# Optimization experiments

Measured on AMD Instinct MI355X. Metric: run time of the kernel, lower is better.

## Reference

```python
import jax, jax.numpy as jnp
import numpy as np

N_HEADS = 16
NEG_BIAS = -1000000000.0


def setup_inputs() -> dict:
    key = jax.random.key(0)
    k1, k2, k3, k4 = jax.random.split(key, 4)
    B, S, D = 2, 2048, 1024
    queries = jax.random.normal(k1, (B, S, D), dtype=jnp.float32)
    keys = jax.random.normal(k2, (B, S, D), dtype=jnp.float32)
    values = jax.random.normal(k3, (B, S, D), dtype=jnp.float32)
    mask = jax.random.randint(k4, (B, S, S), 0, 2, dtype=jnp.int32)
    return {"queries": queries, "keys": keys, "values": values, "mask": mask}


def _split_heads(x):
    B, S, D = x.shape
    return x.reshape(B, S, N_HEADS, D // N_HEADS).transpose(0, 2, 1, 3)  # [B,H,S,d]


def reference(queries, keys, values, mask):
    q = _split_heads(queries)   # [B,H,Sq,d]
    k = _split_heads(keys)      # [B,H,Sk,d]
    v = _split_heads(values)    # [B,H,Sk,d]
    d_head = q.shape[-1]
    # scaled dot product similarity
    sim = jnp.einsum('bhqd,bhkd->bhqk', q, k) / jnp.sqrt(jnp.float32(d_head))
    # additive mask (softmax attention function -> non-hadamard)
    bias = NEG_BIAS * (1.0 - mask.astype(sim.dtype))[:, None]  # [B,1,Sq,Sk]
    sim = sim + bias
    # softmax with max-subtraction (numerically stable, as in original)
    weights = jax.nn.softmax(sim, axis=-1)
    out = jnp.einsum('bhqk,bhkd->bhqd', weights, v)  # [B,H,Sq,d]
    B, H, Sq, d = out.shape
    return out.transpose(0, 2, 1, 3).reshape(B, Sq, H * d)
```

## Files before the change

### kernel.cpp

```cpp
#include <hip/hip_runtime.h>

#define S_LEN 2048
#define D_MODEL 1024
#define DH 64
#define BQ 128
#define BK 128
#define LDK 72
#define LDV 136
#define ZSCALE 0.18033688f

using short8 = __attribute__((ext_vector_type(8))) short;
using s4v    = __attribute__((ext_vector_type(4))) short;
using f32x4  = __attribute__((ext_vector_type(4))) float;

__device__ __forceinline__ unsigned short f2bf(float x) {
    union { float f; unsigned int u; } c; c.f = x;
    unsigned int u = c.u;
    u += 0x7fffu + ((u >> 16) & 1u);
    return (unsigned short)(u >> 16);
}

__global__ __launch_bounds__(256) void cvt_fused(const float* __restrict__ V,
                                                 const int* __restrict__ M,
                                                 const float* __restrict__ K,
                                                 unsigned short* __restrict__ VT,
                                                 unsigned long long* __restrict__ Mb,
                                                 unsigned short* __restrict__ KB) {
    const int blk = blockIdx.x;
    const int tid = threadIdx.x;
    if (blk < 1024) {
        __shared__ float tsF[64][65];
        const int b  = blk >> 9;
        const int h  = (blk >> 5) & 15;
        const int s0 = (blk & 31) * 64;
        #pragma unroll
        for (int it = 0; it < 2; ++it) {
            int seg = tid + it * 256;
            int s = seg >> 3, d8 = (seg & 7) << 3;
            const float* p = V + (size_t)(b * S_LEN + s0 + s) * D_MODEL + h * DH + d8;
            f32x4 a = *(const f32x4*)p;
            f32x4 c = *(const f32x4*)(p + 4);
            #pragma unroll
            for (int j = 0; j < 4; ++j) { tsF[s][d8 + j] = a[j]; tsF[s][d8 + 4 + j] = c[j]; }
        }
        __syncthreads();
        #pragma unroll
        for (int it = 0; it < 2; ++it) {
            int seg = tid + it * 256;
            int d = seg >> 3, s8 = (seg & 7) << 3;
            short8 w;
            #pragma unroll
            for (int j = 0; j < 8; ++j) w[j] = (short)f2bf(tsF[s8 + j][d]);
            *(short8*)(VT + ((size_t)((b * 16 + h) * 64 + d)) * S_LEN + s0 + s8) = w;
        }
    } else if (blk < 2048) {
        const int pb   = blk - 1024;
        const int wave = tid >> 6, lane = tid & 63;
        const int row  = pb * 4 + wave;
        const int* mp  = M + (size_t)row * S_LEN;
        #pragma unroll 4
        for (int it = 0; it < 32; ++it) {
            int m = mp[it * 64 + lane];
            unsigned long long bal = __ballot(m != 0);
            if (lane == 0) Mb[(size_t)row * 32 + it] = bal;
        }
    } else {
        size_t base = (size_t)(blk - 2048) * 4096;
        #pragma unroll
        for (int it = 0; it < 4; ++it) {
            size_t i = base + ((size_t)(it * 256 + tid)) * 4;
            f32x4 a = *(const f32x4*)(K + i);
            s4v w;
            #pragma unroll
            for (int j = 0; j < 4; ++j) w[j] = (short)f2bf(a[j]);
            *(s4v*)(KB + i) = w;
        }
    }
}

__global__ __launch_bounds__(256) void mha_fwd_v11(
    const float* __restrict__ Q,
    const float* __restrict__ K,
    const unsigned short* __restrict__ KB,
    const unsigned short* __restrict__ VT,
    const unsigned long long* __restrict__ Mb,
    float* __restrict__ O,
    int kbf)
{
    __shared__ alignas(16) unsigned short Ks[BK][LDK];
    __shared__ alignas(16) unsigned short Vt[DH][LDV];

    const int blk0 = blockIdx.x;
    const int blk  = ((blk0 & 7) << 6) | (blk0 >> 3);

    const int b   = blk >> 8;
    const int h   = (blk >> 4) & 15;
    const int qbase = (blk & 15) * BQ;
    const int bh  = b * 16 + h;

    const int tid  = threadIdx.x;
    const int wave = tid >> 6;
    const int lane = tid & 63;
    const int n16  = lane & 15;
    const int quad = lane >> 4;
    const int bq   = quad << 3;

    const int srow = tid >> 3, sc8 = (tid & 7) << 3;
    const int prow = (((srow >> 2) & 1) << 4) | (((srow >> 3) & 3) << 2) | (srow & 3);
    const int vrow = tid >> 4, vc8 = (tid & 15) << 3;

    short8 qf[2][2];
    #pragma unroll
    for (int qg = 0; qg < 2; ++qg) {
        const size_t qoff = (size_t)(b * S_LEN + qbase + wave * 32 + qg * 16 + n16) * D_MODEL
                          + h * DH + quad * 8;
        f32x4 a0 = *(const f32x4*)(Q + qoff);
        f32x4 a1 = *(const f32x4*)(Q + qoff + 4);
        f32x4 a2 = *(const f32x4*)(Q + qoff + 32);
        f32x4 a3 = *(const f32x4*)(Q + qoff + 36);
        short8 q0, q1;
        #pragma unroll
        for (int j = 0; j < 4; ++j) {
            q0[j] = (short)f2bf(a0[j] * ZSCALE); q0[4 + j] = (short)f2bf(a1[j] * ZSCALE);
            q1[j] = (short)f2bf(a2[j] * ZSCALE); q1[4 + j] = (short)f2bf(a3[j] * ZSCALE);
        }
        qf[qg][0] = q0; qf[qg][1] = q1;
    }

    const short8 ones = {0x3F80,0x3F80,0x3F80,0x3F80,0x3F80,0x3F80,0x3F80,0x3F80};

    f32x4 o[2][4], o4[2];
    #pragma unroll
    for (int qg = 0; qg < 2; ++qg) {
        #pragma unroll
        for (int dg = 0; dg < 4; ++dg) o[qg][dg] = f32x4{0.f,0.f,0.f,0.f};
        o4[qg] = f32x4{0.f,0.f,0.f,0.f};
    }

    const unsigned long long* mrow[2];
    #pragma unroll
    for (int qg = 0; qg < 2; ++qg)
        mrow[qg] = Mb + (size_t)(b * S_LEN + qbase + wave * 32 + qg * 16 + n16) * 32;

    const size_t kbase = (size_t)(b * S_LEN) * D_MODEL + h * DH;
    const size_t vbase = (size_t)(bh * 64) * S_LEN;

    short8 ka[4], va[4];
    unsigned long long mw[2][2];
    if (kbf) {
        #pragma unroll
        for (int i = 0; i < 4; ++i)
            ka[i] = *(const short8*)(KB + kbase + (size_t)(i * 32 + srow) * D_MODEL + sc8);
    } else {
        #pragma unroll
        for (int i = 0; i < 4; ++i) {
            const float* kp = K + kbase + (size_t)(i * 32 + srow) * D_MODEL + sc8;
            f32x4 p0 = *(const f32x4*)kp, p1 = *(const f32x4*)(kp + 4);
            short8 w;
            #pragma unroll
            for (int j = 0; j < 4; ++j) { w[j] = (short)f2bf(p0[j]); w[4 + j] = (short)f2bf(p1[j]); }
            ka[i] = w;
        }
    }
    #pragma unroll
    for (int i = 0; i < 4; ++i)
        va[i] = *(const short8*)(VT + vbase + (size_t)(vrow + 16 * i) * S_LEN + vc8);
    #pragma unroll
    for (int qg = 0; qg < 2; ++qg) { mw[qg][0] = mrow[qg][0]; mw[qg][1] = mrow[qg][1]; }

    for (int kb = 0; kb < S_LEN; kb += BK) {
        __builtin_amdgcn_s_barrier();
        __builtin_amdgcn_sched_barrier(0);

        #pragma unroll
        for (int i = 0; i < 4; ++i) {
            *(short8*)&Ks[prow + 32 * i][sc8] = ka[i];
            *(short8*)&Vt[vrow + 16 * i][vc8] = va[i];
        }

        const int kn = kb + BK;
        const bool more = kn < S_LEN;
        short8 nka[4], nva[4];
        unsigned long long nmw[2][2];
        if (more) {
            if (kbf) {
                #pragma unroll
                for (int i = 0; i < 4; ++i)
                    nka[i] = *(const short8*)(KB + kbase + (size_t)(kn + i * 32 + srow) * D_MODEL + sc8);
            } else {
                #pragma unroll
                for (int i = 0; i < 4; ++i) {
                    const float* kp = K + kbase + (size_t)(kn + i * 32 + srow) * D_MODEL + sc8;
                    f32x4 p0 = *(const f32x4*)kp, p1 = *(const f32x4*)(kp + 4);
                    short8 w;
                    #pragma unroll
                    for (int j = 0; j < 4; ++j) { w[j] = (short)f2bf(p0[j]); w[4 + j] = (short)f2bf(p1[j]); }
                    nka[i] = w;
                }
            }
            #pragma unroll
            for (int i = 0; i < 4; ++i)
                nva[i] = *(const short8*)(VT + vbase + (size_t)(vrow + 16 * i) * S_LEN + kn + vc8);
            const int wi = kn >> 6;
            #pragma unroll
            for (int qg = 0; qg < 2; ++qg) { nmw[qg][0] = mrow[qg][wi]; nmw[qg][1] = mrow[qg][wi + 1]; }
        }

        asm volatile("s_waitcnt lgkmcnt(0)" ::: "memory");
        __builtin_amdgcn_s_barrier();
        __builtin_amdgcn_sched_barrier(0);

        unsigned int am[2][4];
        #pragma unroll
        for (int qg = 0; qg < 2; ++qg) {
            am[qg][0] = ((unsigned int)mw[qg][0]) >> bq;
            am[qg][1] = ((unsigned int)(mw[qg][0] >> 32)) >> bq;
            am[qg][2] = ((unsigned int)mw[qg][1]) >> bq;
            am[qg][3] = ((unsigned int)(mw[qg][1] >> 32)) >> bq;
        }

        union { unsigned int u[4]; short8 v; } Af[2][4];
        __builtin_amdgcn_s_setprio(1);
        #pragma unroll
        for (int ct = 0; ct < 8; ++ct) {
            short8 kf0 = *(const short8*)&Ks[ct * 16 + n16][     quad * 8];
            short8 kf1 = *(const short8*)&Ks[ct * 16 + n16][32 + quad * 8];
            f32x4 sA = {0.f,0.f,0.f,0.f}, sB = sA;
            sA = __builtin_amdgcn_mfma_f32_16x16x32_bf16(kf0, qf[0][0], sA, 0, 0, 0);
            sA = __builtin_amdgcn_mfma_f32_16x16x32_bf16(kf1, qf[0][1], sA, 0, 0, 0);
            sB = __builtin_amdgcn_mfma_f32_16x16x32_bf16(kf0, qf[1][0], sB, 0, 0, 0);
            sB = __builtin_amdgcn_mfma_f32_16x16x32_bf16(kf1, qf[1][1], sB, 0, 0, 0);
            unsigned int puA[4], puB[4];
            #pragma unroll
            for (int r = 0; r < 4; ++r) {
                puA[r] = __float_as_uint(__builtin_amdgcn_exp2f(sA[r]));
                puB[r] = __float_as_uint(__builtin_amdgcn_exp2f(sB[r]));
            }
            const int sel = ct >> 1, sb = (ct & 1) * 4;
            unsigned int nibA = (am[0][sel] >> sb) & 0xFu;
            unsigned int nibB = (am[1][sel] >> sb) & 0xFu;
            unsigned int m8A = ((nibA * 0x00204081u) & 0x01010101u) * 0xFFu;
            unsigned int m8B = ((nibB * 0x00204081u) & 0x01010101u) * 0xFFu;
            const int kc = ct >> 1, ub = (ct & 1) * 2;
            Af[0][kc].u[ub + 0] = __builtin_amdgcn_perm(puA[1], puA[0], 0x07060302u)
                                & __builtin_amdgcn_perm(0u, m8A, 0x01010000u);
            Af[0][kc].u[ub + 1] = __builtin_amdgcn_perm(puA[3], puA[2], 0x07060302u)
                                & __builtin_amdgcn_perm(0u, m8A, 0x03030202u);
            Af[1][kc].u[ub + 0] = __builtin_amdgcn_perm(puB[1], puB[0], 0x07060302u)
                                & __builtin_amdgcn_perm(0u, m8B, 0x01010000u);
            Af[1][kc].u[ub + 1] = __builtin_amdgcn_perm(puB[3], puB[2], 0x07060302u)
                                & __builtin_amdgcn_perm(0u, m8B, 0x03030202u);
        }

        #pragma unroll
        for (int kc = 0; kc < 4; ++kc) {
            short8 v0 = *(const short8*)&Vt[      n16][kc * 32 + quad * 8];
            short8 v1 = *(const short8*)&Vt[16 + n16][kc * 32 + quad * 8];
            short8 v2 = *(const short8*)&Vt[32 + n16][kc * 32 + quad * 8];
            short8 v3 = *(const short8*)&Vt[48 + n16][kc * 32 + quad * 8];
            #pragma unroll
            for (int qg = 0; qg < 2; ++qg) {
                short8 af = Af[qg][kc].v;
                o[qg][0] = __builtin_amdgcn_mfma_f32_16x16x32_bf16(af, v0, o[qg][0], 0, 0, 0);
                o[qg][1] = __builtin_amdgcn_mfma_f32_16x16x32_bf16(af, v1, o[qg][1], 0, 0, 0);
                o[qg][2] = __builtin_amdgcn_mfma_f32_16x16x32_bf16(af, v2, o[qg][2], 0, 0, 0);
                o[qg][3] = __builtin_amdgcn_mfma_f32_16x16x32_bf16(af, v3, o[qg][3], 0, 0, 0);
                o4[qg]   = __builtin_amdgcn_mfma_f32_16x16x32_bf16(af, ones, o4[qg], 0, 0, 0);
            }
        }
        __builtin_amdgcn_s_setprio(0);

        if (more) {
            #pragma unroll
            for (int i = 0; i < 4; ++i) { ka[i] = nka[i]; va[i] = nva[i]; }
            #pragma unroll
            for (int qg = 0; qg < 2; ++qg) { mw[qg][0] = nmw[qg][0]; mw[qg][1] = nmw[qg][1]; }
        }
    }

    #pragma unroll
    for (int qg = 0; qg < 2; ++qg) {
        #pragma unroll
        for (int r = 0; r < 4; ++r) {
            float rl = 1.f / o4[qg][r];
            size_t row = (size_t)(b * S_LEN + qbase + wave * 32 + qg * 16 + quad * 4 + r);
            float* op = O + row * D_MODEL + h * DH + n16;
            op[0]  = o[qg][0][r] * rl;
            op[16] = o[qg][1][r] * rl;
            op[32] = o[qg][2][r] * rl;
            op[48] = o[qg][3][r] * rl;
        }
    }
}

extern "C" void kernel_launch(void* const* d_in, const int* in_sizes, int n_in,
                              void* d_out, int out_size, void* d_ws, size_t ws_size,
                              hipStream_t stream) {
    const float* Q = (const float*)d_in[0];
    const float* K = (const float*)d_in[1];
    const float* V = (const float*)d_in[2];
    const int*   M = (const int*)d_in[3];
    float*       O = (float*)d_out;

    const size_t NEL = (size_t)2 * S_LEN * D_MODEL;
    const size_t VT_BYTES = NEL * sizeof(unsigned short);
    const size_t KB_BYTES = NEL * sizeof(unsigned short);
    const size_t MB_BYTES = (size_t)2 * S_LEN * 32 * 8;

    if (ws_size >= VT_BYTES + KB_BYTES + MB_BYTES) {
        unsigned short* VT = (unsigned short*)d_ws;
        unsigned short* KB = (unsigned short*)((char*)d_ws + VT_BYTES);
        unsigned long long* Mb = (unsigned long long*)((char*)d_ws + VT_BYTES + KB_BYTES);
        hipLaunchKernelGGL(cvt_fused, dim3(3072), dim3(256), 0, stream, V, M, K, VT, Mb, KB);
        hipLaunchKernelGGL(mha_fwd_v11, dim3(512), dim3(256), 0, stream,
                           Q, K, KB, VT, Mb, O, 1);
    } else {
        unsigned short* VT = (unsigned short*)d_ws;
        unsigned long long* Mb = (unsigned long long*)((char*)d_ws + VT_BYTES);
        hipLaunchKernelGGL(cvt_fused, dim3(2048), dim3(256), 0, stream, V, M, K, VT, Mb, (unsigned short*)0);
        hipLaunchKernelGGL(mha_fwd_v11, dim3(512), dim3(256), 0, stream,
                           Q, K, (const unsigned short*)0, VT, Mb, O, 0);
    }
}
```

Baseline: 171.3 us.

## Load K fragments directly to registers and double-buffer V in LDS

Drops the shared-memory K tile. Each wave now loads its K MFMA fragments straight from global memory into registers, using a row permutation that matches the old LDS layout, and prefetches the next tile after the QK stage. V goes into a two-stage LDS buffer, which lets the loop drop one of its two barriers per iteration. This removes LDS traffic and a barrier for K. In exchange, each wave redundantly reads the whole K tile from global/L2 (4x duplication across waves) and register pressure rises from holding 16 short8 K fragments.

```diff
diff --git a/kernel.cpp b/kernel.cpp
--- a/kernel.cpp
+++ b/kernel.cpp
@@ -5,7 +5,6 @@
 #define DH 64
 #define BQ 128
 #define BK 128
-#define LDK 72
 #define LDV 136
 #define ZSCALE 0.18033688f
 
@@ -78,7 +77,7 @@
     }
 }
 
-__global__ __launch_bounds__(256) void mha_fwd_v11(
+__global__ __launch_bounds__(256) void mha_fwd_v12(
     const float* __restrict__ Q,
     const float* __restrict__ K,
     const unsigned short* __restrict__ KB,
@@ -87,8 +86,7 @@
     float* __restrict__ O,
     int kbf)
 {
-    __shared__ alignas(16) unsigned short Ks[BK][LDK];
-    __shared__ alignas(16) unsigned short Vt[DH][LDV];
+    __shared__ alignas(16) unsigned short Vt[2][DH][LDV];
 
     const int blk0 = blockIdx.x;
     const int blk  = ((blk0 & 7) << 6) | (blk0 >> 3);
@@ -104,9 +102,8 @@
     const int n16  = lane & 15;
     const int quad = lane >> 4;
     const int bq   = quad << 3;
-
-    const int srow = tid >> 3, sc8 = (tid & 7) << 3;
-    const int prow = (((srow >> 2) & 1) << 4) | (((srow >> 3) & 3) << 2) | (srow & 3);
+    const int lrow = ((n16 >> 2) << 3) | (n16 & 3);
+
     const int vrow = tid >> 4, vc8 = (tid & 15) << 3;
 
     short8 qf[2][2];
@@ -145,59 +142,51 @@
     const size_t kbase = (size_t)(b * S_LEN) * D_MODEL + h * DH;
     const size_t vbase = (size_t)(bh * 64) * S_LEN;
 
-    short8 ka[4], va[4];
+    short8 kf[8][2];
+    auto load_kf = [&](int kt) {
+        #pragma unroll
+        for (int ct = 0; ct < 8; ++ct) {
+            const int cst  = ((ct >> 2) << 6) | (((ct >> 1) & 1) << 5) | ((ct & 1) << 2);
+            const int crow = kt + cst + lrow;
+            if (kbf) {
+                const unsigned short* kp = KB + kbase + (size_t)crow * D_MODEL + quad * 8;
+                kf[ct][0] = *(const short8*)kp;
+                kf[ct][1] = *(const short8*)(kp + 32);
+            } else {
+                const float* kp = K + kbase + (size_t)crow * D_MODEL + quad * 8;
+                f32x4 p0 = *(const f32x4*)kp,        p1 = *(const f32x4*)(kp + 4);
+                f32x4 p2 = *(const f32x4*)(kp + 32), p3 = *(const f32x4*)(kp + 36);
+                short8 w0, w1;
+                #pragma unroll
+                for (int j = 0; j < 4; ++j) {
+                    w0[j] = (short)f2bf(p0[j]); w0[4 + j] = (short)f2bf(p1[j]);
+                    w1[j] = (short)f2bf(p2[j]); w1[4 + j] = (short)f2bf(p3[j]);
+                }
+                kf[ct][0] = w0; kf[ct][1] = w1;
+            }
+        }
+    };
+
+    short8 va[4];
     unsigned long long mw[2][2];
-    if (kbf) {
-        #pragma unroll
-        for (int i = 0; i < 4; ++i)
-            ka[i] = *(const short8*)(KB + kbase + (size_t)(i * 32 + srow) * D_MODEL + sc8);
-    } else {
-        #pragma unroll
-        for (int i = 0; i < 4; ++i) {
-            const float* kp = K + kbase + (size_t)(i * 32 + srow) * D_MODEL + sc8;
-            f32x4 p0 = *(const f32x4*)kp, p1 = *(const f32x4*)(kp + 4);
-            short8 w;
-            #pragma unroll
-            for (int j = 0; j < 4; ++j) { w[j] = (short)f2bf(p0[j]); w[4 + j] = (short)f2bf(p1[j]); }
-            ka[i] = w;
-        }
-    }
     #pragma unroll
     for (int i = 0; i < 4; ++i)
         va[i] = *(const short8*)(VT + vbase + (size_t)(vrow + 16 * i) * S_LEN + vc8);
+    load_kf(0);
     #pragma unroll
     for (int qg = 0; qg < 2; ++qg) { mw[qg][0] = mrow[qg][0]; mw[qg][1] = mrow[qg][1]; }
 
-    for (int kb = 0; kb < S_LEN; kb += BK) {
-        __builtin_amdgcn_s_barrier();
-        __builtin_amdgcn_sched_barrier(0);
-
-        #pragma unroll
-        for (int i = 0; i < 4; ++i) {
-            *(short8*)&Ks[prow + 32 * i][sc8] = ka[i];
-            *(short8*)&Vt[vrow + 16 * i][vc8] = va[i];
-        }
+    int p = 0;
+    for (int kb = 0; kb < S_LEN; kb += BK, p ^= 1) {
+        #pragma unroll
+        for (int i = 0; i < 4; ++i)
+            *(short8*)&Vt[p][vrow + 16 * i][vc8] = va[i];
 
         const int kn = kb + BK;
         const bool more = kn < S_LEN;
-        short8 nka[4], nva[4];
+        short8 nva[4];
         unsigned long long nmw[2][2];
         if (more) {
-            if (kbf) {
-                #pragma unroll
-                for (int i = 0; i < 4; ++i)
-                    nka[i] = *(const short8*)(KB + kbase + (size_t)(kn + i * 32 + srow) * D_MODEL + sc8);
-            } else {
-                #pragma unroll
-                for (int i = 0; i < 4; ++i) {
-                    const float* kp = K + kbase + (size_t)(kn + i * 32 + srow) * D_MODEL + sc8;
-                    f32x4 p0 = *(const f32x4*)kp, p1 = *(const f32x4*)(kp + 4);
-                    short8 w;
-                    #pragma unroll
-                    for (int j = 0; j < 4; ++j) { w[j] = (short)f2bf(p0[j]); w[4 + j] = (short)f2bf(p1[j]); }
-                    nka[i] = w;
-                }
-            }
             #pragma unroll
             for (int i = 0; i < 4; ++i)
                 nva[i] = *(const short8*)(VT + vbase + (size_t)(vrow + 16 * i) * S_LEN + kn + vc8);
@@ -205,10 +194,6 @@
             #pragma unroll
             for (int qg = 0; qg < 2; ++qg) { nmw[qg][0] = mrow[qg][wi]; nmw[qg][1] = mrow[qg][wi + 1]; }
         }
-
-        asm volatile("s_waitcnt lgkmcnt(0)" ::: "memory");
-        __builtin_amdgcn_s_barrier();
-        __builtin_amdgcn_sched_barrier(0);
 
         unsigned int am[2][4];
         #pragma unroll
@@ -223,13 +208,11 @@
         __builtin_amdgcn_s_setprio(1);
         #pragma unroll
         for (int ct = 0; ct < 8; ++ct) {
-            short8 kf0 = *(const short8*)&Ks[ct * 16 + n16][     quad * 8];
-            short8 kf1 = *(const short8*)&Ks[ct * 16 + n16][32 + quad * 8];
             f32x4 sA = {0.f,0.f,0.f,0.f}, sB = sA;
-            sA = __builtin_amdgcn_mfma_f32_16x16x32_bf16(kf0, qf[0][0], sA, 0, 0, 0);
-            sA = __builtin_amdgcn_mfma_f32_16x16x32_bf16(kf1, qf[0][1], sA, 0, 0, 0);
-            sB = __builtin_amdgcn_mfma_f32_16x16x32_bf16(kf0, qf[1][0], sB, 0, 0, 0);
-            sB = __builtin_amdgcn_mfma_f32_16x16x32_bf16(kf1, qf[1][1], sB, 0, 0, 0);
+            sA = __builtin_amdgcn_mfma_f32_16x16x32_bf16(kf[ct][0], qf[0][0], sA, 0, 0, 0);
+            sA = __builtin_amdgcn_mfma_f32_16x16x32_bf16(kf[ct][1], qf[0][1], sA, 0, 0, 0);
+            sB = __builtin_amdgcn_mfma_f32_16x16x32_bf16(kf[ct][0], qf[1][0], sB, 0, 0, 0);
+            sB = __builtin_amdgcn_mfma_f32_16x16x32_bf16(kf[ct][1], qf[1][1], sB, 0, 0, 0);
             unsigned int puA[4], puB[4];
             #pragma unroll
             for (int r = 0; r < 4; ++r) {
@@ -251,13 +234,21 @@
             Af[1][kc].u[ub + 1] = __builtin_amdgcn_perm(puB[3], puB[2], 0x07060302u)
                                 & __builtin_amdgcn_perm(0u, m8B, 0x03030202u);
         }
-
+        __builtin_amdgcn_s_setprio(0);
+
+        asm volatile("s_waitcnt lgkmcnt(0)" ::: "memory");
+        __builtin_amdgcn_s_barrier();
+        __builtin_amdgcn_sched_barrier(0);
+
+        if (more) load_kf(kn);
+
+        __builtin_amdgcn_s_setprio(1);
         #pragma unroll
         for (int kc = 0; kc < 4; ++kc) {
-            short8 v0 = *(const short8*)&Vt[      n16][kc * 32 + quad * 8];
-            short8 v1 = *(const short8*)&Vt[16 + n16][kc * 32 + quad * 8];
-            short8 v2 = *(const short8*)&Vt[32 + n16][kc * 32 + quad * 8];
-            short8 v3 = *(const short8*)&Vt[48 + n16][kc * 32 + quad * 8];
+            short8 v0 = *(const short8*)&Vt[p][      n16][kc * 32 + quad * 8];
+            short8 v1 = *(const short8*)&Vt[p][16 + n16][kc * 32 + quad * 8];
+            short8 v2 = *(const short8*)&Vt[p][32 + n16][kc * 32 + quad * 8];
+            short8 v3 = *(const short8*)&Vt[p][48 + n16][kc * 32 + quad * 8];
             #pragma unroll
             for (int qg = 0; qg < 2; ++qg) {
                 short8 af = Af[qg][kc].v;
@@ -272,7 +263,7 @@
 
         if (more) {
             #pragma unroll
-            for (int i = 0; i < 4; ++i) { ka[i] = nka[i]; va[i] = nva[i]; }
+            for (int i = 0; i < 4; ++i) va[i] = nva[i];
             #pragma unroll
             for (int qg = 0; qg < 2; ++qg) { mw[qg][0] = nmw[qg][0]; mw[qg][1] = nmw[qg][1]; }
         }
@@ -312,13 +303,13 @@
         unsigned short* KB = (unsigned short*)((char*)d_ws + VT_BYTES);
         unsigned long long* Mb = (unsigned long long*)((char*)d_ws + VT_BYTES + KB_BYTES);
         hipLaunchKernelGGL(cvt_fused, dim3(3072), dim3(256), 0, stream, V, M, K, VT, Mb, KB);
-        hipLaunchKernelGGL(mha_fwd_v11, dim3(512), dim3(256), 0, stream,
+        hipLaunchKernelGGL(mha_fwd_v12, dim3(512), dim3(256), 0, stream,
                            Q, K, KB, VT, Mb, O, 1);
     } else {
         unsigned short* VT = (unsigned short*)d_ws;
         unsigned long long* Mb = (unsigned long long*)((char*)d_ws + VT_BYTES);
         hipLaunchKernelGGL(cvt_fused, dim3(2048), dim3(256), 0, stream, V, M, K, VT, Mb, (unsigned short*)0);
-        hipLaunchKernelGGL(mha_fwd_v11, dim3(512), dim3(256), 0, stream,
+        hipLaunchKernelGGL(mha_fwd_v12, dim3(512), dim3(256), 0, stream,
                            Q, K, (const unsigned short*)0, VT, Mb, O, 0);
     }
 }
```

New measurement: 214.6 us. 1.25x slower.

## Software-pipeline QK and PV across tiles with double-buffered LDS

Applied to the files above, without the earlier changes.

Double-buffers the K and V shared-memory tiles. The PV MFMAs of tile t-1 are interleaved with the QK and exp work of tile t, so matrix-core and VALU/transcendental work can overlap within a wave. The main loop is manually unrolled by two, with ping-pong register sets for K/V/mask prefetch and for the probability fragments. This doubles LDS use and raises register pressure, which could lower occupancy or cause spills.

```diff
diff --git a/kernel.cpp b/kernel.cpp
--- a/kernel.cpp
+++ b/kernel.cpp
@@ -5,6 +5,7 @@
 #define DH 64
 #define BQ 128
 #define BK 128
+#define NT (S_LEN / BK)
 #define LDK 72
 #define LDV 136
 #define ZSCALE 0.18033688f
@@ -12,6 +13,9 @@
 using short8 = __attribute__((ext_vector_type(8))) short;
 using s4v    = __attribute__((ext_vector_type(4))) short;
 using f32x4  = __attribute__((ext_vector_type(4))) float;
+using u32x4  = __attribute__((ext_vector_type(4))) unsigned int;
+
+#define BMM(a, b, c) __builtin_amdgcn_mfma_f32_16x16x32_bf16((a), (b), (c), 0, 0, 0)
 
 __device__ __forceinline__ unsigned short f2bf(float x) {
     union { float f; unsigned int u; } c; c.f = x;
@@ -78,7 +82,7 @@
     }
 }
 
-__global__ __launch_bounds__(256) void mha_fwd_v11(
+__global__ __launch_bounds__(256) void mha_fwd_v13(
     const float* __restrict__ Q,
     const float* __restrict__ K,
     const unsigned short* __restrict__ KB,
@@ -87,8 +91,8 @@
     float* __restrict__ O,
     int kbf)
 {
-    __shared__ alignas(16) unsigned short Ks[BK][LDK];
-    __shared__ alignas(16) unsigned short Vt[DH][LDV];
+    __shared__ alignas(16) unsigned short Ks[2][BK][LDK];
+    __shared__ alignas(16) unsigned short Vt[2][DH][LDV];
 
     const int blk0 = blockIdx.x;
     const int blk  = ((blk0 & 7) << 6) | (blk0 >> 3);
@@ -145,72 +149,45 @@
     const size_t kbase = (size_t)(b * S_LEN) * D_MODEL + h * DH;
     const size_t vbase = (size_t)(bh * 64) * S_LEN;
 
-    short8 ka[4], va[4];
-    unsigned long long mw[2][2];
-    if (kbf) {
+    short8 kaA[4], vaA[4], kaB[4], vaB[4];
+    unsigned long long mwA[2][2], mwB[2][2];
+    u32x4 AfA[2][4], AfB[2][4];
+
+    auto LOADKV = [&](int kb2, short8 (&ka)[4], short8 (&va)[4]) {
+        if (kb2 >= S_LEN) return;
+        if (kbf) {
+            #pragma unroll
+            for (int i = 0; i < 4; ++i)
+                ka[i] = *(const short8*)(KB + kbase + (size_t)(kb2 + i * 32 + srow) * D_MODEL + sc8);
+        } else {
+            #pragma unroll
+            for (int i = 0; i < 4; ++i) {
+                const float* kp = K + kbase + (size_t)(kb2 + i * 32 + srow) * D_MODEL + sc8;
+                f32x4 p0 = *(const f32x4*)kp, p1 = *(const f32x4*)(kp + 4);
+                short8 w;
+                #pragma unroll
+                for (int j = 0; j < 4; ++j) { w[j] = (short)f2bf(p0[j]); w[4 + j] = (short)f2bf(p1[j]); }
+                ka[i] = w;
+            }
+        }
         #pragma unroll
         for (int i = 0; i < 4; ++i)
-            ka[i] = *(const short8*)(KB + kbase + (size_t)(i * 32 + srow) * D_MODEL + sc8);
-    } else {
+            va[i] = *(const short8*)(VT + vbase + (size_t)(vrow + 16 * i) * S_LEN + kb2 + vc8);
+    };
+    auto LOADM = [&](int kb2, unsigned long long (&mw)[2][2]) {
+        if (kb2 >= S_LEN) return;
+        const int wi = kb2 >> 6;
+        #pragma unroll
+        for (int qg = 0; qg < 2; ++qg) { mw[qg][0] = mrow[qg][wi]; mw[qg][1] = mrow[qg][wi + 1]; }
+    };
+    auto STAGE = [&](int pb, short8 (&ka)[4], short8 (&va)[4]) {
         #pragma unroll
         for (int i = 0; i < 4; ++i) {
-            const float* kp = K + kbase + (size_t)(i * 32 + srow) * D_MODEL + sc8;
-            f32x4 p0 = *(const f32x4*)kp, p1 = *(const f32x4*)(kp + 4);
-            short8 w;
-            #pragma unroll
-            for (int j = 0; j < 4; ++j) { w[j] = (short)f2bf(p0[j]); w[4 + j] = (short)f2bf(p1[j]); }
-            ka[i] = w;
-        }
-    }
-    #pragma unroll
-    for (int i = 0; i < 4; ++i)
-        va[i] = *(const short8*)(VT + vbase + (size_t)(vrow + 16 * i) * S_LEN + vc8);
-    #pragma unroll
-    for (int qg = 0; qg < 2; ++qg) { mw[qg][0] = mrow[qg][0]; mw[qg][1] = mrow[qg][1]; }
-
-    for (int kb = 0; kb < S_LEN; kb += BK) {
-        __builtin_amdgcn_s_barrier();
-        __builtin_amdgcn_sched_barrier(0);
-
-        #pragma unroll
-        for (int i = 0; i < 4; ++i) {
-            *(short8*)&Ks[prow + 32 * i][sc8] = ka[i];
-            *(short8*)&Vt[vrow + 16 * i][vc8] = va[i];
-        }
-
-        const int kn = kb + BK;
-        const bool more = kn < S_LEN;
-        short8 nka[4], nva[4];
-        unsigned long long nmw[2][2];
-        if (more) {
-            if (kbf) {
-                #pragma unroll
-                for (int i = 0; i < 4; ++i)
-                    nka[i] = *(const short8*)(KB + kbase + (size_t)(kn + i * 32 + srow) * D_MODEL + sc8);
-            } else {
-                #pragma unroll
-                for (int i = 0; i < 4; ++i) {
-                    const float* kp = K + kbase + (size_t)(kn + i * 32 + srow) * D_MODEL + sc8;
-                    f32x4 p0 = *(const f32x4*)kp, p1 = *(const f32x4*)(kp + 4);
-                    short8 w;
-                    #pragma unroll
-                    for (int j = 0; j < 4; ++j) { w[j] = (short)f2bf(p0[j]); w[4 + j] = (short)f2bf(p1[j]); }
-                    nka[i] = w;
-                }
-            }
-            #pragma unroll
-            for (int i = 0; i < 4; ++i)
-                nva[i] = *(const short8*)(VT + vbase + (size_t)(vrow + 16 * i) * S_LEN + kn + vc8);
-            const int wi = kn >> 6;
-            #pragma unroll
-            for (int qg = 0; qg < 2; ++qg) { nmw[qg][0] = mrow[qg][wi]; nmw[qg][1] = mrow[qg][wi + 1]; }
-        }
-
-        asm volatile("s_waitcnt lgkmcnt(0)" ::: "memory");
-        __builtin_amdgcn_s_barrier();
-        __builtin_amdgcn_sched_barrier(0);
-
-        unsigned int am[2][4];
+            *(short8*)&Ks[pb][prow + 32 * i][sc8] = ka[i];
+            *(short8*)&Vt[pb][vrow + 16 * i][vc8] = va[i];
+        }
+    };
+    auto MKAM = [&](unsigned long long (&mw)[2][2], unsigned int (&am)[2][4]) {
         #pragma unroll
         for (int qg = 0; qg < 2; ++qg) {
             am[qg][0] = ((unsigned int)mw[qg][0]) >> bq;
@@ -218,64 +195,108 @@
             am[qg][2] = ((unsigned int)mw[qg][1]) >> bq;
             am[qg][3] = ((unsigned int)(mw[qg][1] >> 32)) >> bq;
         }
-
-        union { unsigned int u[4]; short8 v; } Af[2][4];
+    };
+    auto QKCT = [&](int pb, int ct, unsigned int (&am)[2][4], u32x4 (&Af)[2][4]) {
+        short8 kf0 = *(const short8*)&Ks[pb][ct * 16 + n16][     quad * 8];
+        short8 kf1 = *(const short8*)&Ks[pb][ct * 16 + n16][32 + quad * 8];
+        f32x4 sA = {0.f,0.f,0.f,0.f}, sB = sA;
+        sA = BMM(kf0, qf[0][0], sA); sA = BMM(kf1, qf[0][1], sA);
+        sB = BMM(kf0, qf[1][0], sB); sB = BMM(kf1, qf[1][1], sB);
+        unsigned int puA[4], puB[4];
+        #pragma unroll
+        for (int r = 0; r < 4; ++r) {
+            puA[r] = __float_as_uint(__builtin_amdgcn_exp2f(sA[r]));
+            puB[r] = __float_as_uint(__builtin_amdgcn_exp2f(sB[r]));
+        }
+        const int sel = ct >> 1, sb = (ct & 1) * 4, kc = ct >> 1, ub = (ct & 1) * 2;
+        unsigned int nibA = (am[0][sel] >> sb) & 0xFu;
+        unsigned int nibB = (am[1][sel] >> sb) & 0xFu;
+        unsigned int m8A = ((nibA * 0x00204081u) & 0x01010101u) * 0xFFu;
+        unsigned int m8B = ((nibB * 0x00204081u) & 0x01010101u) * 0xFFu;
+        Af[0][kc][ub + 0] = __builtin_amdgcn_perm(puA[1], puA[0], 0x07060302u)
+                          & __builtin_amdgcn_perm(0u, m8A, 0x01010000u);
+        Af[0][kc][ub + 1] = __builtin_amdgcn_perm(puA[3], puA[2], 0x07060302u)
+                          & __builtin_amdgcn_perm(0u, m8A, 0x03030202u);
+        Af[1][kc][ub + 0] = __builtin_amdgcn_perm(puB[1], puB[0], 0x07060302u)
+                          & __builtin_amdgcn_perm(0u, m8B, 0x01010000u);
+        Af[1][kc][ub + 1] = __builtin_amdgcn_perm(puB[3], puB[2], 0x07060302u)
+                          & __builtin_amdgcn_perm(0u, m8B, 0x03030202u);
+    };
+    auto PVKC = [&](int pb, int kc, u32x4 (&Af)[2][4]) {
+        short8 v0 = *(const short8*)&Vt[pb][      n16][kc * 32 + quad * 8];
+        short8 v1 = *(const short8*)&Vt[pb][16 + n16][kc * 32 + quad * 8];
+        short8 v2 = *(const short8*)&Vt[pb][32 + n16][kc * 32 + quad * 8];
+        short8 v3 = *(const short8*)&Vt[pb][48 + n16][kc * 32 + quad * 8];
+        union { u32x4 u; short8 s; } c0, c1;
+        c0.u = Af[0][kc]; c1.u = Af[1][kc];
+        o[0][0] = BMM(c0.s, v0, o[0][0]); o[0][1] = BMM(c0.s, v1, o[0][1]);
+        o[0][2] = BMM(c0.s, v2, o[0][2]); o[0][3] = BMM(c0.s, v3, o[0][3]);
+        o4[0]   = BMM(c0.s, ones, o4[0]);
+        o[1][0] = BMM(c1.s, v0, o[1][0]); o[1][1] = BMM(c1.s, v1, o[1][1]);
+        o[1][2] = BMM(c1.s, v2, o[1][2]); o[1][3] = BMM(c1.s, v3, o[1][3]);
+        o4[1]   = BMM(c1.s, ones, o4[1]);
+    };
+    auto COMPUTE = [&](int qb, int vb, unsigned int (&am)[2][4],
+                       u32x4 (&AfC)[2][4], u32x4 (&AfP)[2][4], bool doPV) {
         __builtin_amdgcn_s_setprio(1);
-        #pragma unroll
-        for (int ct = 0; ct < 8; ++ct) {
-            short8 kf0 = *(const short8*)&Ks[ct * 16 + n16][     quad * 8];
-            short8 kf1 = *(const short8*)&Ks[ct * 16 + n16][32 + quad * 8];
-            f32x4 sA = {0.f,0.f,0.f,0.f}, sB = sA;
-            sA = __builtin_amdgcn_mfma_f32_16x16x32_bf16(kf0, qf[0][0], sA, 0, 0, 0);
-            sA = __builtin_amdgcn_mfma_f32_16x16x32_bf16(kf1, qf[0][1], sA, 0, 0, 0);
-            sB = __builtin_amdgcn_mfma_f32_16x16x32_bf16(kf0, qf[1][0], sB, 0, 0, 0);
-            sB = __builtin_amdgcn_mfma_f32_16x16x32_bf16(kf1, qf[1][1], sB, 0, 0, 0);
-            unsigned int puA[4], puB[4];
-            #pragma unroll
-            for (int r = 0; r < 4; ++r) {
-                puA[r] = __float_as_uint(__builtin_amdgcn_exp2f(sA[r]));
-                puB[r] = __float_as_uint(__builtin_amdgcn_exp2f(sB[r]));
-            }
-            const int sel = ct >> 1, sb = (ct & 1) * 4;
-            unsigned int nibA = (am[0][sel] >> sb) & 0xFu;
-            unsigned int nibB = (am[1][sel] >> sb) & 0xFu;
-            unsigned int m8A = ((nibA * 0x00204081u) & 0x01010101u) * 0xFFu;
-            unsigned int m8B = ((nibB * 0x00204081u) & 0x01010101u) * 0xFFu;
-            const int kc = ct >> 1, ub = (ct & 1) * 2;
-            Af[0][kc].u[ub + 0] = __builtin_amdgcn_perm(puA[1], puA[0], 0x07060302u)
-                                & __builtin_amdgcn_perm(0u, m8A, 0x01010000u);
-            Af[0][kc].u[ub + 1] = __builtin_amdgcn_perm(puA[3], puA[2], 0x07060302u)
-                                & __builtin_amdgcn_perm(0u, m8A, 0x03030202u);
-            Af[1][kc].u[ub + 0] = __builtin_amdgcn_perm(puB[1], puB[0], 0x07060302u)
-                                & __builtin_amdgcn_perm(0u, m8B, 0x01010000u);
-            Af[1][kc].u[ub + 1] = __builtin_amdgcn_perm(puB[3], puB[2], 0x07060302u)
-                                & __builtin_amdgcn_perm(0u, m8B, 0x03030202u);
-        }
-
-        #pragma unroll
-        for (int kc = 0; kc < 4; ++kc) {
-            short8 v0 = *(const short8*)&Vt[      n16][kc * 32 + quad * 8];
-            short8 v1 = *(const short8*)&Vt[16 + n16][kc * 32 + quad * 8];
-            short8 v2 = *(const short8*)&Vt[32 + n16][kc * 32 + quad * 8];
-            short8 v3 = *(const short8*)&Vt[48 + n16][kc * 32 + quad * 8];
-            #pragma unroll
-            for (int qg = 0; qg < 2; ++qg) {
-                short8 af = Af[qg][kc].v;
-                o[qg][0] = __builtin_amdgcn_mfma_f32_16x16x32_bf16(af, v0, o[qg][0], 0, 0, 0);
-                o[qg][1] = __builtin_amdgcn_mfma_f32_16x16x32_bf16(af, v1, o[qg][1], 0, 0, 0);
-                o[qg][2] = __builtin_amdgcn_mfma_f32_16x16x32_bf16(af, v2, o[qg][2], 0, 0, 0);
-                o[qg][3] = __builtin_amdgcn_mfma_f32_16x16x32_bf16(af, v3, o[qg][3], 0, 0, 0);
-                o4[qg]   = __builtin_amdgcn_mfma_f32_16x16x32_bf16(af, ones, o4[qg], 0, 0, 0);
-            }
-        }
+        QKCT(qb, 0, am, AfC); QKCT(qb, 1, am, AfC); if (doPV) PVKC(vb, 0, AfP);
+        QKCT(qb, 2, am, AfC); QKCT(qb, 3, am, AfC); if (doPV) PVKC(vb, 1, AfP);
+        QKCT(qb, 4, am, AfC); QKCT(qb, 5, am, AfC); if (doPV) PVKC(vb, 2, AfP);
+        QKCT(qb, 6, am, AfC); QKCT(qb, 7, am, AfC); if (doPV) PVKC(vb, 3, AfP);
         __builtin_amdgcn_s_setprio(0);
-
-        if (more) {
-            #pragma unroll
-            for (int i = 0; i < 4; ++i) { ka[i] = nka[i]; va[i] = nva[i]; }
-            #pragma unroll
-            for (int qg = 0; qg < 2; ++qg) { mw[qg][0] = nmw[qg][0]; mw[qg][1] = nmw[qg][1]; }
-        }
+    };
+
+    LOADKV(0, kaA, vaA); LOADM(0, mwA);
+    STAGE(0, kaA, vaA);
+    LOADKV(BK, kaB, vaB); LOADM(BK, mwB);
+    asm volatile("s_waitcnt lgkmcnt(0)" ::: "memory");
+    __builtin_amdgcn_s_barrier();
+    __builtin_amdgcn_sched_barrier(0);
+
+    {
+        unsigned int am[2][4]; MKAM(mwA, am);
+        COMPUTE(0, 0, am, AfA, AfB, false);
+        LOADM(2 * BK, mwA);
+        STAGE(1, kaB, vaB);
+        LOADKV(2 * BK, kaA, vaA);
+        asm volatile("s_waitcnt lgkmcnt(0)" ::: "memory");
+        __builtin_amdgcn_s_barrier();
+        __builtin_amdgcn_sched_barrier(0);
+    }
+
+    for (int t = 1; t <= 13; t += 2) {
+        {
+            unsigned int am[2][4]; MKAM(mwB, am);
+            COMPUTE(1, 0, am, AfB, AfA, true);
+            LOADM((t + 2) * BK, mwB);
+            __builtin_amdgcn_s_barrier();
+            __builtin_amdgcn_sched_barrier(0);
+            STAGE(0, kaA, vaA);
+            LOADKV((t + 2) * BK, kaB, vaB);
+            asm volatile("s_waitcnt lgkmcnt(0)" ::: "memory");
+            __builtin_amdgcn_s_barrier();
+            __builtin_amdgcn_sched_barrier(0);
+        }
+        {
+            unsigned int am[2][4]; MKAM(mwA, am);
+            COMPUTE(0, 1, am, AfA, AfB, true);
+            LOADM((t + 3) * BK, mwA);
+            __builtin_amdgcn_s_barrier();
+            __builtin_amdgcn_sched_barrier(0);
+            STAGE(1, kaB, vaB);
+            LOADKV((t + 3) * BK, kaA, vaA);
+            asm volatile("s_waitcnt lgkmcnt(0)" ::: "memory");
+            __builtin_amdgcn_s_barrier();
+            __builtin_amdgcn_sched_barrier(0);
+        }
+    }
+
+    {
+        unsigned int am[2][4]; MKAM(mwB, am);
+        COMPUTE(1, 0, am, AfB, AfA, true);
+        __builtin_amdgcn_s_setprio(1);
+        PVKC(1, 0, AfB); PVKC(1, 1, AfB); PVKC(1, 2, AfB); PVKC(1, 3, AfB);
+        __builtin_amdgcn_s_setprio(0);
     }
 
     #pragma unroll
@@ -312,13 +333,13 @@
         unsigned short* KB = (unsigned short*)((char*)d_ws + VT_BYTES);
         unsigned long long* Mb = (unsigned long long*)((char*)d_ws + VT_BYTES + KB_BYTES);
         hipLaunchKernelGGL(cvt_fused, dim3(3072), dim3(256), 0, stream, V, M, K, VT, Mb, KB);
-        hipLaunchKernelGGL(mha_fwd_v11, dim3(512), dim3(256), 0, stream,
+        hipLaunchKernelGGL(mha_fwd_v13, dim3(512), dim3(256), 0, stream,
                            Q, K, KB, VT, Mb, O, 1);
     } else {
         unsigned short* VT = (unsigned short*)d_ws;
         unsigned long long* Mb = (unsigned long long*)((char*)d_ws + VT_BYTES);
         hipLaunchKernelGGL(cvt_fused, dim3(2048), dim3(256), 0, stream, V, M, K, VT, Mb, (unsigned short*)0);
-        hipLaunchKernelGGL(mha_fwd_v11, dim3(512), dim3(256), 0, stream,
+        hipLaunchKernelGGL(mha_fwd_v13, dim3(512), dim3(256), 0, stream,
                            Q, K, (const unsigned short*)0, VT, Mb, O, 0);
     }
 }
```

New measurement: 188.5 us. +10.1%, slower.
